# Kernel optimization log

Hardware: AMD Instinct MI355X
Metric: run time of the kernel (lower is better)

The kernel has to match this reference:

```python
import jax, jax.numpy as jnp
import numpy as np

LN_EPS = 1e-6
KERNEL_EPS = 1e-3  # fast_attention generalized kernel_epsilon


def layer_norm(x, scale, bias):
    mu = jnp.mean(x, axis=-1, keepdims=True)
    var = jnp.mean(jnp.square(x - mu), axis=-1, keepdims=True)
    return (x - mu) * jax.lax.rsqrt(var + LN_EPS) * scale + bias


def sinusoidal_pos_emb(seq_len, dim):
    pos = jnp.arange(seq_len, dtype=jnp.float32)[:, None]
    div = jnp.exp(jnp.arange(0, dim, 2, dtype=jnp.float32) * (-np.log(10000.0) / dim))
    pe = jnp.zeros((seq_len, dim), dtype=jnp.float32)
    pe = pe.at[:, 0::2].set(jnp.sin(pos * div)).at[:, 1::2].set(jnp.cos(pos * div))
    return pe


def favor_generalized_attention(x, mask, wq, wk, wv, wo):
    # x: [B,S,E], mask: [B,S,1] (1 for real tokens), wq/wk/wv: [E,H,D], wo: [H,D,E]
    q = jnp.einsum('bse,ehd->bshd', x, wq)
    k = jnp.einsum('bse,ehd->bshd', x, wk)
    v = jnp.einsum('bse,ehd->bshd', x, wv)
    # deterministic generalized features: phi(x) = relu(x) + eps
    phi_q = jax.nn.relu(q) + KERNEL_EPS
    phi_k = (jax.nn.relu(k) + KERNEL_EPS) * mask[..., None]  # zero padded keys
    # bidirectional linear attention: O(S * H * D^2)
    kv = jnp.einsum('bshm,bshd->bhmd', phi_k, v)      # [B,H,D,D]
    z = jnp.sum(phi_k, axis=1)                        # [B,H,D]
    num = jnp.einsum('bshm,bhmd->bshd', phi_q, kv)    # [B,S,H,D]
    den = jnp.einsum('bshm,bhm->bsh', phi_q, z)       # [B,S,H]
    out = num / den[..., None]
    return jnp.einsum('bshd,hde->bse', out, wo)


def setup_inputs() -> dict:
    key = jax.random.key(0)
    B, S, V, E, H, D, M, L = 4, 4096, 32000, 512, 8, 64, 2048, 6
    ks = jax.random.split(key, 8)
    w_scale = 0.02
    return {
        'inputs': jax.random.randint(ks[0], (B, S), 0, V, dtype=jnp.int32),
        'embed': jax.random.normal(ks[1], (V, E), jnp.float32),
        'ln1_scale': jnp.ones((L, E), jnp.float32),
        'ln1_bias': jnp.zeros((L, E), jnp.float32),
        'wq': jax.random.normal(ks[2], (L, E, H, D), jnp.float32) * w_scale,
        'wk': jax.random.normal(ks[3], (L, E, H, D), jnp.float32) * w_scale,
        'wv': jax.random.normal(ks[4], (L, E, H, D), jnp.float32) * w_scale,
        'wo': jax.random.normal(ks[5], (L, H, D, E), jnp.float32) * w_scale,
        'ln2_scale': jnp.ones((L, E), jnp.float32),
        'ln2_bias': jnp.zeros((L, E), jnp.float32),
        'w1': jax.random.normal(ks[6], (L, E, M), jnp.float32) * w_scale,
        'b1': jnp.zeros((L, M), jnp.float32),
        'w2': jax.random.normal(ks[7], (L, M, E), jnp.float32) * w_scale,
        'b2': jnp.zeros((L, E), jnp.float32),
        'lnf_scale': jnp.ones((E,), jnp.float32),
        'lnf_bias': jnp.zeros((E,), jnp.float32),
    }


def reference(inputs, embed, ln1_scale, ln1_bias, wq, wk, wv, wo,
              ln2_scale, ln2_bias, w1, b1, w2, b2, lnf_scale, lnf_bias):
    B, S = inputs.shape
    E = embed.shape[1]
    L = wq.shape[0]
    mask = (inputs > 0).astype(embed.dtype)[..., None]  # [B,S,1] padding mask
    x = embed[inputs]                                   # [B,S,E]
    x = x + sinusoidal_pos_emb(S, E)[None]
    for l in range(L):
        h = layer_norm(x, ln1_scale[l], ln1_bias[l])
        h = favor_generalized_attention(h, mask, wq[l], wk[l], wv[l], wo[l])
        x = x + h
        y = layer_norm(x, ln2_scale[l], ln2_bias[l])
        y = jax.nn.gelu(y @ w1[l] + b1[l]) @ w2[l] + b2[l]
        x = x + y
    return layer_norm(x, lnf_scale, lnf_bias)
```

## Files before the change

kernel.cpp:

```cpp
#include <hip/hip_runtime.h>
#include <hip/hip_bf16.h>

#define BATCH 4
#define SEQ   4096
#define BS_TOK (BATCH*SEQ)
#define EMB   512
#define NH    8
#define HD    64
#define FF    2048
#define NL    6

typedef unsigned short u16;
typedef __attribute__((ext_vector_type(8))) short bf16x8;
typedef __attribute__((ext_vector_type(4))) float f32x4;

__device__ __forceinline__ float bf2f(u16 u) {
    union { unsigned int i; float f; } x; x.i = ((unsigned int)u) << 16; return x.f;
}
__device__ __forceinline__ u16 f2bf(float f) {
    __hip_bfloat16 b = __float2bfloat16(f);
    return *(u16*)&b;
}
__device__ __forceinline__ float gelu_fast(float x) {
    float e = __expf(x * (-1.5957691216057308f - 0.0713548162726009f * x * x));
    return x * __builtin_amdgcn_rcpf(1.f + e);
}
__device__ __forceinline__ void store_out(float* p, float v) { *p = v; }
__device__ __forceinline__ void store_out(u16* p, float v) { *p = f2bf(v); }
__device__ __forceinline__ void store_pair(float* p, float a, float b) {
    *(float2*)p = make_float2(a, b);
}
__device__ __forceinline__ void store_pair(u16* p, float a, float b) {
    unsigned int u = ((unsigned int)f2bf(b) << 16) | (unsigned int)f2bf(a);
    *(unsigned int*)p = u;
}

__device__ __forceinline__ void gl_lds16(const void* g, void* l) {
    __builtin_amdgcn_global_load_lds(
        (__attribute__((address_space(1))) void*)g,
        (__attribute__((address_space(3))) void*)l, 16, 0, 0);
}

__global__ __launch_bounds__(128) void embed_kernel(
        const int* __restrict__ tok, const float* __restrict__ emb,
        float* __restrict__ X, float* __restrict__ maskf) {
    int row = blockIdx.x;
    int t = threadIdx.x;
    int id = tok[row];
    if (t == 0) maskf[row] = (id > 0) ? 1.f : 0.f;
    int s = row & (SEQ - 1);
    int e0 = t * 4;
    float4 u = *(const float4*)(emb + (size_t)id * EMB + e0);
    float vals[4] = { u.x, u.y, u.z, u.w };
    float out[4];
#pragma unroll
    for (int j = 0; j < 4; ++j) {
        int ee = e0 + j;
        int i = ee >> 1;
        float div = expf(-0.035977892078031970f * (float)i);
        float ang = (float)s * div;
        float pe = (ee & 1) ? cosf(ang) : sinf(ang);
        out[j] = vals[j] + pe;
    }
    *(float4*)(X + (size_t)row * EMB + e0) = make_float4(out[0], out[1], out[2], out[3]);
}

template<typename OUT>
__global__ __launch_bounds__(256) void ln_kernel(
        const float* __restrict__ X, const float* __restrict__ sc,
        const float* __restrict__ bi, OUT* __restrict__ Y) {
    int row = blockIdx.x, t = threadIdx.x;
    const float* x = X + (size_t)row * EMB;
    float2 v = *(const float2*)(x + 2 * t);
    float a = v.x, b = v.y;
    float s = a + b, q = a * a + b * b;
#pragma unroll
    for (int off = 32; off; off >>= 1) {
        s += __shfl_xor(s, off);
        q += __shfl_xor(q, off);
    }
    __shared__ float ss[4], qq[4];
    int w = t >> 6;
    if ((t & 63) == 0) { ss[w] = s; qq[w] = q; }
    __syncthreads();
    s = ss[0] + ss[1] + ss[2] + ss[3];
    q = qq[0] + qq[1] + qq[2] + qq[3];
    float mu = s * (1.f / 512.f);
    float var = q * (1.f / 512.f) - mu * mu;
    float rstd = rsqrtf(var + 1e-6f);
    float2 scv = *(const float2*)(sc + 2 * t);
    float2 biv = *(const float2*)(bi + 2 * t);
    float y0 = (a - mu) * rstd * scv.x + biv.x;
    float y1 = (b - mu) * rstd * scv.y + biv.y;
    store_pair(&Y[(size_t)row * EMB + 2 * t], y0, y1);
}

__global__ __launch_bounds__(256) void transpose_w(
        const float* __restrict__ W0, const float* __restrict__ W1,
        const float* __restrict__ W2, const float* __restrict__ W3,
        u16* __restrict__ WT, int K, int N) {
    const float* W = (blockIdx.z == 0) ? W0 : (blockIdx.z == 1) ? W1
                   : (blockIdx.z == 2) ? W2 : W3;
    u16* dst = WT + (size_t)blockIdx.z * K * N;
    __shared__ u16 tile[32][33];
    int n0 = blockIdx.x * 32, k0 = blockIdx.y * 32;
    int tx = threadIdx.x & 31, ty = threadIdx.x >> 5;
#pragma unroll
    for (int u = 0; u < 4; ++u)
        tile[ty + u * 8][tx] = f2bf(W[(size_t)(k0 + ty + u * 8) * N + n0 + tx]);
    __syncthreads();
#pragma unroll
    for (int u = 0; u < 4; ++u)
        dst[(size_t)(n0 + ty + u * 8) * K + k0 + tx] = tile[tx][ty + u * 8];
}

template<int OP, typename OUT>
__global__ __launch_bounds__(256, 4) void mfma_gemm(
        const u16* __restrict__ A, const u16* __restrict__ BT,
        const float* __restrict__ bias, const float* __restrict__ rowscale,
        const float* __restrict__ residual, OUT* __restrict__ C,
        int K, int lda, int ldb, int ldc) {
    __shared__ u16 As[2][128 * 32];
    __shared__ u16 Bs[2][128 * 32];
    int tid = threadIdx.x;
    int wid = tid >> 6, lane = tid & 63;
    int nwg = gridDim.x * gridDim.y;
    int lin = blockIdx.y * gridDim.x + blockIdx.x;
    int swz = (nwg & 7) ? lin : ((lin & 7) * (nwg >> 3) + (lin >> 3));
    int bx = swz % gridDim.x, by = swz / gridDim.x;
    int row0 = by * 128, col0 = bx * 128;
    int wm = (wid & 1) * 64, wn = (wid >> 1) * 64;
    int quad = lane >> 4, l16 = lane & 15;

    f32x4 acc[4][4];
#pragma unroll
    for (int i = 0; i < 4; ++i)
#pragma unroll
        for (int j = 0; j < 4; ++j)
#pragma unroll
            for (int r = 0; r < 4; ++r) acc[i][j][r] = 0.f;

    int rsub = lane >> 2;
    int koff = (lane & 3) * 8;
    const u16* gA = A  + (size_t)(row0 + wid * 16 + rsub) * lda + koff;
    const u16* gB = BT + (size_t)(col0 + wid * 16 + rsub) * ldb + koff;

    auto stage = [&](int bb, int kk) {
        u16* lA = As[bb] + wid * 512;
        u16* lB = Bs[bb] + wid * 512;
#pragma unroll
        for (int i = 0; i < 2; ++i) {
            gl_lds16(gA + (size_t)(i * 64) * lda + kk, lA + i * 2048);
            gl_lds16(gB + (size_t)(i * 64) * ldb + kk, lB + i * 2048);
        }
    };

    int nt = K >> 5;
    stage(0, 0);
    __syncthreads();
    for (int t = 0; t < nt; ++t) {
        int cur = t & 1;
        if (t + 1 < nt) stage(cur ^ 1, (t + 1) * 32);
        bf16x8 af[4], bfv[4];
#pragma unroll
        for (int i = 0; i < 4; ++i)
            af[i] = *(const bf16x8*)(As[cur] + (wm + i * 16 + l16) * 32 + quad * 8);
#pragma unroll
        for (int j = 0; j < 4; ++j)
            bfv[j] = *(const bf16x8*)(Bs[cur] + (wn + j * 16 + l16) * 32 + quad * 8);
#pragma unroll
        for (int i = 0; i < 4; ++i)
#pragma unroll
            for (int j = 0; j < 4; ++j)
                acc[i][j] = __builtin_amdgcn_mfma_f32_16x16x32_bf16(af[i], bfv[j], acc[i][j], 0, 0, 0);
        __syncthreads();
    }

    int seg = col0 >> 9;
    float bc[4];
#pragma unroll
    for (int j = 0; j < 4; ++j)
        bc[j] = bias ? bias[col0 + wn + j * 16 + l16] : 0.f;
#pragma unroll
    for (int i = 0; i < 4; ++i) {
        float res[4][4];
        if (residual) {
#pragma unroll
            for (int r = 0; r < 4; ++r) {
                size_t rb = (size_t)(row0 + wm + i * 16 + quad * 4 + r) * ldc + col0 + wn;
#pragma unroll
                for (int j = 0; j < 4; ++j)
                    res[r][j] = residual[rb + j * 16 + l16];
            }
        }
#pragma unroll
        for (int r = 0; r < 4; ++r) {
            int row = row0 + wm + i * 16 + quad * 4 + r;
            float rsv = (OP == 3 && seg == 1) ? rowscale[row] : 1.f;
            size_t rb = (size_t)row * ldc + col0 + wn;
#pragma unroll
            for (int j = 0; j < 4; ++j) {
                float val = acc[i][j][r] + bc[j];
                if (OP == 1) val = gelu_fast(val);
                if (OP == 3 && seg < 2) val = fmaxf(val, 0.f) + 1e-3f;
                if (OP == 3 && seg == 1) val *= rsv;
                size_t idx = rb + j * 16 + l16;
                if (residual) val += res[r][j];
                store_out(&C[idx], val);
            }
        }
    }
}

__global__ __launch_bounds__(256) void kv_reduce_mfma(
        const u16* __restrict__ PK, const u16* __restrict__ V,
        float* __restrict__ KV, float* __restrict__ Z, int ld) {
    __shared__ __align__(16) u16 pks[32][68];
    __shared__ __align__(16) u16 vvs[32][68];
    int bh = blockIdx.x;
    int b = bh >> 3, hh = bh & 7;
    int cc = blockIdx.y;
    int t = threadIdx.x;
    int wid = t >> 6, lane = t & 63;
    int quad = lane >> 4, l16 = lane & 15;
    int wm = (wid & 1) * 32, wd = (wid >> 1) * 32;

    f32x4 acc[2][2];
    f32x4 zacc[2];
#pragma unroll
    for (int i = 0; i < 2; ++i) {
#pragma unroll
        for (int j = 0; j < 2; ++j)
#pragma unroll
            for (int r = 0; r < 4; ++r) acc[i][j][r] = 0.f;
#pragma unroll
        for (int r = 0; r < 4; ++r) zacc[i][r] = 0.f;
    }
    bf16x8 ones;
#pragma unroll
    for (int e = 0; e < 8; ++e) ones[e] = (short)0x3F80;

    int s_l = t >> 3, mo = (t & 7) * 8;
    const u16* gP = PK + (size_t)(b * SEQ + cc * 256 + s_l) * ld + hh * 64 + mo;
    const u16* gV = V  + (size_t)(b * SEQ + cc * 256 + s_l) * ld + hh * 64 + mo;
    ushort4 p0 = *(const ushort4*)gP;
    ushort4 p1 = *(const ushort4*)(gP + 4);
    ushort4 q0 = *(const ushort4*)gV;
    ushort4 q1 = *(const ushort4*)(gV + 4);

    for (int st = 0; st < 8; ++st) {
        *(ushort4*)&pks[s_l][mo]     = p0;
        *(ushort4*)&pks[s_l][mo + 4] = p1;
        *(ushort4*)&vvs[s_l][mo]     = q0;
        *(ushort4*)&vvs[s_l][mo + 4] = q1;
        __syncthreads();
        if (st < 7) {
            gP += (size_t)32 * ld;  gV += (size_t)32 * ld;
            p0 = *(const ushort4*)gP;  p1 = *(const ushort4*)(gP + 4);
            q0 = *(const ushort4*)gV;  q1 = *(const ushort4*)(gV + 4);
        }
        bf16x8 af[2], bfv[2];
#pragma unroll
        for (int i = 0; i < 2; ++i) {
#pragma unroll
            for (int e = 0; e < 8; ++e) {
                af[i][e]  = (short)pks[quad * 8 + e][wm + i * 16 + l16];
                bfv[i][e] = (short)vvs[quad * 8 + e][wd + i * 16 + l16];
            }
        }
#pragma unroll
        for (int i = 0; i < 2; ++i)
#pragma unroll
            for (int j = 0; j < 2; ++j)
                acc[i][j] = __builtin_amdgcn_mfma_f32_16x16x32_bf16(af[i], bfv[j], acc[i][j], 0, 0, 0);
        if (wid < 2) {
            zacc[0] = __builtin_amdgcn_mfma_f32_16x16x32_bf16(af[0], ones, zacc[0], 0, 0, 0);
            zacc[1] = __builtin_amdgcn_mfma_f32_16x16x32_bf16(af[1], ones, zacc[1], 0, 0, 0);
        }
        __syncthreads();
    }

#pragma unroll
    for (int i = 0; i < 2; ++i)
#pragma unroll
        for (int j = 0; j < 2; ++j)
#pragma unroll
            for (int r = 0; r < 4; ++r)
                atomicAdd(&KV[((size_t)bh * 64 + wm + i * 16 + quad * 4 + r) * 64
                              + wd + j * 16 + l16], acc[i][j][r]);
    if (wid < 2 && l16 == 0) {
#pragma unroll
        for (int i = 0; i < 2; ++i)
#pragma unroll
            for (int r = 0; r < 4; ++r)
                atomicAdd(&Z[(size_t)bh * 64 + wm + i * 16 + quad * 4 + r], zacc[i][r]);
    }
}

__global__ __launch_bounds__(256) void attn_out2(
        const u16* __restrict__ PQ, const float* __restrict__ KV,
        const float* __restrict__ Z, u16* __restrict__ O, int ld) {
    __shared__ float kvT[64 * 65];
    __shared__ float zsh[64];
    __shared__ float phs[4][72];
    int hh = blockIdx.y;
    int row0 = blockIdx.x * 32;
    int b = row0 >> 12;
    int bh = b * NH + hh;
    int t = threadIdx.x;
    const float* kvg = KV + (size_t)bh * 4096;
#pragma unroll
    for (int u = 0; u < 16; ++u) {
        int idx = u * 256 + t;
        kvT[(idx & 63) * 65 + (idx >> 6)] = kvg[idx];
    }
    if (t < 64) zsh[t] = Z[(size_t)bh * 64 + t];
    __syncthreads();
    int wid = t >> 6, lane = t & 63;
    const float* kvrow = kvT + lane * 65;
    for (int rr = 0; rr < 8; ++rr) {
        int row = row0 + wid * 8 + rr;
        float p = bf2f(PQ[(size_t)row * ld + hh * 64 + lane]);
        float d = p * zsh[lane];
#pragma unroll
        for (int off = 32; off; off >>= 1) d += __shfl_xor(d, off);
        d = fmaxf(d, 1e-20f);
        phs[wid][lane] = p;
        float acc = 0.f;
#pragma unroll
        for (int mm = 0; mm < 64; ++mm)
            acc = fmaf(phs[wid][mm], kvrow[mm], acc);
        O[(size_t)row * EMB + hh * 64 + lane] = f2bf(acc / d);
    }
}

extern "C" void kernel_launch(void* const* d_in, const int* in_sizes, int n_in,
                              void* d_out, int out_size, void* d_ws, size_t ws_size,
                              hipStream_t stream) {
    (void)in_sizes; (void)n_in; (void)out_size; (void)ws_size;
    const int*   tok  = (const int*)d_in[0];
    const float* emb  = (const float*)d_in[1];
    const float* ln1s = (const float*)d_in[2];
    const float* ln1b = (const float*)d_in[3];
    const float* wq   = (const float*)d_in[4];
    const float* wk   = (const float*)d_in[5];
    const float* wv   = (const float*)d_in[6];
    const float* wo   = (const float*)d_in[7];
    const float* ln2s = (const float*)d_in[8];
    const float* ln2b = (const float*)d_in[9];
    const float* w1   = (const float*)d_in[10];
    const float* b1   = (const float*)d_in[11];
    const float* w2   = (const float*)d_in[12];
    const float* b2   = (const float*)d_in[13];
    const float* lnfs = (const float*)d_in[14];
    const float* lnfb = (const float*)d_in[15];

    char* ws = (char*)d_ws;
    const size_t MB = 1024 * 1024;
    float* x    = (float*)(ws);
    u16*   h    = (u16*)(ws + 32 * MB);
    u16*   qkv  = (u16*)(ws + 48 * MB);
    u16*   m    = qkv;
    float* kv   = (float*)(ws + 112 * MB);
    float* z    = kv + BATCH * NH * HD * HD;
    float* maskf = (float*)(ws + 112 * MB + 768 * 1024);
    u16*   wt   = (u16*)(ws + 113 * MB);
    u16*   w1t  = (u16*)(ws + 115 * MB);
    u16*   w2t  = (u16*)(ws + 117 * MB);

    embed_kernel<<<BS_TOK, 128, 0, stream>>>(tok, emb, x, maskf);

    const size_t WSTEP = (size_t)EMB * EMB;
    dim3 gQKV(12, BS_TOK / 128);
    dim3 gN512(4, BS_TOK / 128);
    dim3 gN2048(16, BS_TOK / 128);

    for (int l = 0; l < NL; ++l) {
        ln_kernel<u16><<<BS_TOK, 256, 0, stream>>>(x, ln1s + l * EMB, ln1b + l * EMB, h);
        transpose_w<<<dim3(16, 16, 4), 256, 0, stream>>>(
            wq + l * WSTEP, wk + l * WSTEP, wv + l * WSTEP, wo + l * WSTEP, wt, EMB, EMB);
        mfma_gemm<3, u16><<<gQKV, 256, 0, stream>>>(
            h, wt, nullptr, maskf, nullptr, qkv, EMB, EMB, EMB, 1536);

        hipMemsetAsync(kv, 0, (size_t)(BATCH * NH * HD * HD + BATCH * NH * HD) * sizeof(float), stream);
        kv_reduce_mfma<<<dim3(BATCH * NH, SEQ / 256), 256, 0, stream>>>(qkv + 512, qkv + 1024, kv, z, 1536);
        attn_out2<<<dim3(BS_TOK / 32, NH), 256, 0, stream>>>(qkv, kv, z, h, 1536);

        mfma_gemm<0, float><<<gN512, 256, 0, stream>>>(
            h, wt + 3 * WSTEP, nullptr, nullptr, x, x, EMB, EMB, EMB, EMB);

        ln_kernel<u16><<<BS_TOK, 256, 0, stream>>>(x, ln2s + l * EMB, ln2b + l * EMB, h);
        const float* w1l = w1 + (size_t)l * EMB * FF;
        const float* w2l = w2 + (size_t)l * FF * EMB;
        const float* b1l = b1 + (size_t)l * FF;
        const float* b2l = b2 + (size_t)l * EMB;
        transpose_w<<<dim3(64, 16, 1), 256, 0, stream>>>(w1l, w1l, w1l, w1l, w1t, EMB, FF);
        transpose_w<<<dim3(16, 64, 1), 256, 0, stream>>>(w2l, w2l, w2l, w2l, w2t, FF, EMB);
        mfma_gemm<1, u16><<<gN2048, 256, 0, stream>>>(
            h, w1t, b1l, nullptr, nullptr, m, EMB, EMB, EMB, FF);
        mfma_gemm<0, float><<<gN512, 256, 0, stream>>>(
            m, w2t, b2l, nullptr, x, x, FF, FF, FF, EMB);
    }

    ln_kernel<float><<<BS_TOK, 256, 0, stream>>>(x, lnfs, lnfb, (float*)d_out);
}
```

Baseline: 1.650 ms.

## Add 256x256-tile 512-thread MFMA GEMM for QKV and FF1 projections

Adds a new GEMM kernel with 256x256 output tiles, 8 waves, a double-buffered direct global-to-LDS load pipeline with explicit vmcnt waits, setprio around MFMA bursts, and a grouped block swizzle. It is used for the QKV projection and the first FFN layer, where K=512, replacing the 128-row kernel. The aim is more operand reuse per tile and better overlap of loads with MFMA work. The trade-offs are heavier register and LDS use (launch_bounds 512,2), fewer blocks per grid, and a hardcoded K of 512 (NKT=8).

```diff
diff --git a/kernel.cpp b/kernel.cpp
--- a/kernel.cpp
+++ b/kernel.cpp
@@ -206,6 +206,121 @@
                 if (OP == 3 && seg == 1) val *= rsv;
                 size_t idx = rb + j * 16 + l16;
                 if (residual) val += res[r][j];
+                store_out(&C[idx], val);
+            }
+        }
+    }
+}
+
+template<int OP, typename OUT>
+__global__ __launch_bounds__(512, 2) void mfma_gemm_big(
+        const u16* __restrict__ A, const u16* __restrict__ BT,
+        const float* __restrict__ bias, const float* __restrict__ rowscale,
+        const float* __restrict__ residual, OUT* __restrict__ C,
+        int lda, int ldb, int ldc) {
+    constexpr int NKT = 8;
+    __shared__ u16 As[2][2 * 256 * 32];
+    __shared__ u16 Bs[2][2 * 256 * 32];
+    int tid = threadIdx.x;
+    int wid = tid >> 6, lane = tid & 63;
+    int nwg = gridDim.x * gridDim.y;
+    int lin = blockIdx.y * gridDim.x + blockIdx.x;
+    int swz = (nwg & 7) ? lin : ((lin & 7) * (nwg >> 3) + (lin >> 3));
+    int bx = swz % gridDim.x, by = swz / gridDim.x;
+    int row0 = by * 256, col0 = bx * 256;
+    int wm = (wid & 1) * 128;
+    int wn = (wid >> 1) * 64;
+    int quad = lane >> 4, l16 = lane & 15;
+
+    f32x4 acc[8][4];
+#pragma unroll
+    for (int i = 0; i < 8; ++i)
+#pragma unroll
+        for (int j = 0; j < 4; ++j)
+#pragma unroll
+            for (int r = 0; r < 4; ++r) acc[i][j][r] = 0.f;
+
+    int srow = tid >> 2;
+    int skp  = (tid & 3) * 8;
+    const u16* gA = A  + (size_t)(row0 + srow) * lda + skp;
+    const u16* gB = BT + (size_t)(col0 + srow) * ldb + skp;
+
+    auto stage = [&](u16* lA, u16* lB, int k0) {
+#pragma unroll
+        for (int pl = 0; pl < 2; ++pl)
+#pragma unroll
+            for (int hf = 0; hf < 2; ++hf) {
+                int ldsoff = pl * 8192 + hf * 4096 + tid * 8;
+                gl_lds16(gA + (size_t)(hf * 128) * lda + k0 + pl * 32, lA + ldsoff);
+                gl_lds16(gB + (size_t)(hf * 128) * ldb + k0 + pl * 32, lB + ldsoff);
+            }
+    };
+
+    auto iter = [&](const u16* lA, const u16* lB, u16* sA, u16* sB, int kt) {
+        if (kt < NKT - 1) asm volatile("s_waitcnt vmcnt(8)" ::: "memory");
+        else              asm volatile("s_waitcnt vmcnt(0)" ::: "memory");
+        __builtin_amdgcn_s_barrier();
+        asm volatile("" ::: "memory");
+        bf16x8 bfv[4][2];
+#pragma unroll
+        for (int nf = 0; nf < 4; ++nf)
+#pragma unroll
+            for (int p = 0; p < 2; ++p)
+                bfv[nf][p] = *(const bf16x8*)(lB + p * 8192 + (wn + nf * 16 + l16) * 32 + quad * 8);
+#pragma unroll
+        for (int q = 0; q < 4; ++q) {
+            bf16x8 af[2][2];
+#pragma unroll
+            for (int mf = 0; mf < 2; ++mf)
+#pragma unroll
+                for (int p = 0; p < 2; ++p)
+                    af[mf][p] = *(const bf16x8*)(lA + p * 8192 + (wm + (q * 2 + mf) * 16 + l16) * 32 + quad * 8);
+            __builtin_amdgcn_s_setprio(1);
+#pragma unroll
+            for (int mf = 0; mf < 2; ++mf)
+#pragma unroll
+                for (int nf = 0; nf < 4; ++nf) {
+                    acc[q * 2 + mf][nf] = __builtin_amdgcn_mfma_f32_16x16x32_bf16(
+                        af[mf][0], bfv[nf][0], acc[q * 2 + mf][nf], 0, 0, 0);
+                    acc[q * 2 + mf][nf] = __builtin_amdgcn_mfma_f32_16x16x32_bf16(
+                        af[mf][1], bfv[nf][1], acc[q * 2 + mf][nf], 0, 0, 0);
+                }
+            __builtin_amdgcn_s_setprio(0);
+        }
+        asm volatile("" ::: "memory");
+        __builtin_amdgcn_s_barrier();
+        asm volatile("" ::: "memory");
+        if (kt + 2 < NKT) stage(sA, sB, (kt + 2) * 64);
+    };
+
+    stage(As[0], Bs[0], 0);
+    stage(As[1], Bs[1], 64);
+#pragma unroll 1
+    for (int kt = 0; kt < NKT; kt += 2) {
+        iter(As[0], Bs[0], As[0], Bs[0], kt);
+        iter(As[1], Bs[1], As[1], Bs[1], kt + 1);
+    }
+
+    int seg = col0 >> 9;
+    float bc[4];
+#pragma unroll
+    for (int nf = 0; nf < 4; ++nf)
+        bc[nf] = bias ? bias[col0 + wn + nf * 16 + l16] : 0.f;
+#pragma unroll
+    for (int ifr = 0; ifr < 8; ++ifr) {
+#pragma unroll
+        for (int r = 0; r < 4; ++r) {
+            int row = row0 + wm + ifr * 16 + quad * 4 + r;
+            float rsv = (OP == 3 && seg == 1) ? rowscale[row] : 1.f;
+            size_t rb = (size_t)row * ldc + col0 + wn;
+#pragma unroll
+            for (int nf = 0; nf < 4; ++nf) {
+                float val = acc[ifr][nf][r] + bc[nf];
+                if (OP == 1) val = gelu_fast(val);
+                if (OP == 3 && seg < 2) val = fmaxf(val, 0.f) + 1e-3f;
+                if (OP == 3 && seg == 1) val *= rsv;
+                size_t idx = rb + nf * 16 + l16;
+                if (residual) val += residual[idx];
                 store_out(&C[idx], val);
             }
         }
@@ -371,16 +486,16 @@
     embed_kernel<<<BS_TOK, 128, 0, stream>>>(tok, emb, x, maskf);
 
     const size_t WSTEP = (size_t)EMB * EMB;
-    dim3 gQKV(12, BS_TOK / 128);
+    dim3 gQKVb(6, BS_TOK / 256);
+    dim3 gFF1b(8, BS_TOK / 256);
     dim3 gN512(4, BS_TOK / 128);
-    dim3 gN2048(16, BS_TOK / 128);
 
     for (int l = 0; l < NL; ++l) {
         ln_kernel<u16><<<BS_TOK, 256, 0, stream>>>(x, ln1s + l * EMB, ln1b + l * EMB, h);
         transpose_w<<<dim3(16, 16, 4), 256, 0, stream>>>(
             wq + l * WSTEP, wk + l * WSTEP, wv + l * WSTEP, wo + l * WSTEP, wt, EMB, EMB);
-        mfma_gemm<3, u16><<<gQKV, 256, 0, stream>>>(
-            h, wt, nullptr, maskf, nullptr, qkv, EMB, EMB, EMB, 1536);
+        mfma_gemm_big<3, u16><<<gQKVb, 512, 0, stream>>>(
+            h, wt, nullptr, maskf, nullptr, qkv, EMB, EMB, 1536);
 
         hipMemsetAsync(kv, 0, (size_t)(BATCH * NH * HD * HD + BATCH * NH * HD) * sizeof(float), stream);
         kv_reduce_mfma<<<dim3(BATCH * NH, SEQ / 256), 256, 0, stream>>>(qkv + 512, qkv + 1024, kv, z, 1536);
@@ -396,8 +511,8 @@
         const float* b2l = b2 + (size_t)l * EMB;
         transpose_w<<<dim3(64, 16, 1), 256, 0, stream>>>(w1l, w1l, w1l, w1l, w1t, EMB, FF);
         transpose_w<<<dim3(16, 64, 1), 256, 0, stream>>>(w2l, w2l, w2l, w2l, w2t, FF, EMB);
-        mfma_gemm<1, u16><<<gN2048, 256, 0, stream>>>(
-            h, w1t, b1l, nullptr, nullptr, m, EMB, EMB, EMB, FF);
+        mfma_gemm_big<1, u16><<<gFF1b, 512, 0, stream>>>(
+            h, w1t, b1l, nullptr, nullptr, m, EMB, EMB, FF);
         mfma_gemm<0, float><<<gN512, 256, 0, stream>>>(
             m, w2t, b2l, nullptr, x, x, FF, FF, FF, EMB);
     }
```

After: 1.773 ms. 7.5% more time.
